# Kernel optimization log

Hardware: AMD Instinct MI355X
Metric: run time of the kernel (lower is better)

## Reference

```python
import jax, jax.numpy as jnp
import numpy as np

IN_F = 512
OUT_F = 512
ALPHA = 0.2   # LeakyReLU negative slope
NEG_INF = -9e15


def setup_inputs() -> dict:
    key = jax.random.key(0)
    k1, k2, k3, k4 = jax.random.split(key, 4)
    B, S = 8, 2048
    hidden_state = jax.random.normal(k1, (B, S, IN_F), dtype=jnp.float32)
    adjacent_matrix = jax.random.uniform(k2, (B, S, S), dtype=jnp.float32)
    # nn.Linear weight (no bias): stored as [out, in] in torch; we keep [in, out] for x @ W
    bound = 1.0 / np.sqrt(IN_F)
    W = jax.random.uniform(k3, (IN_F, OUT_F), dtype=jnp.float32, minval=-bound, maxval=bound)
    # xavier_uniform with gain=1.414 on a: shape [2*out, 1]
    a_bound = 1.414 * np.sqrt(6.0 / (2 * OUT_F + 1))
    a = jax.random.uniform(k4, (2 * OUT_F, 1), dtype=jnp.float32, minval=-a_bound, maxval=a_bound)
    return {"hidden_state": hidden_state, "adjacent_matrix": adjacent_matrix, "W": W, "a": a}


def reference(hidden_state, adjacent_matrix, W, a):
    # Wh: [B, S, out]
    Wh = jnp.einsum('bsi,io->bso', hidden_state, W)
    # additive attention: Wh1 + Wh2^T -> [B, S, S]
    Wh1 = Wh @ a[:OUT_F, :]            # [B, S, 1]
    Wh2 = Wh @ a[OUT_F:, :]            # [B, S, 1]
    e = Wh1 + jnp.swapaxes(Wh2, 1, 2)  # [B, S, S]
    e = jax.nn.leaky_relu(e, negative_slope=ALPHA)
    attention = jnp.where(adjacent_matrix > 0.5, e, NEG_INF)
    # NOTE: original softmaxes over dim=1 (the *row* index), faithfully reproduced
    attention = jax.nn.softmax(attention, axis=1)
    # dropout is identity at inference (training=False)
    h_prime = jnp.einsum('bst,bto->bso', attention, Wh)
    return jax.nn.elu(h_prime)  # concat=True path
```

## Files before the change

### kernel.cpp

```cpp
#include <hip/hip_runtime.h>
#include <hip/hip_bf16.h>
#include <stdint.h>

#define SDIM 2048
#define BDIM 8
#define FDIM 512
constexpr float ALPHA = 0.2f;

typedef __attribute__((ext_vector_type(8))) short bf16x8;
typedef __attribute__((ext_vector_type(4))) float f32x4;

__device__ __forceinline__ unsigned short f2bf(float x) {
  __hip_bfloat16 h = __float2bfloat16(x);
  return *reinterpret_cast<unsigned short*>(&h);
}

__device__ __forceinline__ void gload_lds16(const void* g, void* l) {
  __builtin_amdgcn_global_load_lds(
      (const __attribute__((address_space(1))) unsigned int*)(uintptr_t)g,
      (__attribute__((address_space(3))) unsigned int*)(uintptr_t)l,
      16, 0, 0);
}

__global__ void k0_prep(const float* __restrict__ W, const float* __restrict__ a,
                        float* __restrict__ wa, __hip_bfloat16* __restrict__ WT) {
  int i = blockIdx.x;
  int lane = threadIdx.x;
  float s1 = 0.f, s2 = 0.f;
  for (int o = lane; o < FDIM; o += 64) {
    float w = W[i * FDIM + o];
    s1 += w * a[o];
    s2 += w * a[FDIM + o];
    WT[o * FDIM + i] = __float2bfloat16(w);
  }
  #pragma unroll
  for (int off = 32; off > 0; off >>= 1) {
    s1 += __shfl_down(s1, off);
    s2 += __shfl_down(s2, off);
  }
  if (lane == 0) { wa[i] = s1; wa[FDIM + i] = s2; }
}

__global__ __launch_bounds__(256) void k1_rows(const float* __restrict__ H,
                                               const float* __restrict__ wa,
                                               float* __restrict__ Wh1, float* __restrict__ Wh2,
                                               __hip_bfloat16* __restrict__ Hb) {
  int wid = threadIdx.x >> 6, lane = threadIdx.x & 63;
  long r = (long)blockIdx.x * 4 + wid;
  const float* hr = H + r * FDIM;
  float4 v0 = ((const float4*)hr)[lane];
  float4 v1 = ((const float4*)hr)[lane + 64];
  float4 wa10 = ((const float4*)wa)[lane];
  float4 wa11 = ((const float4*)wa)[lane + 64];
  float4 wa20 = ((const float4*)(wa + FDIM))[lane];
  float4 wa21 = ((const float4*)(wa + FDIM))[lane + 64];
  float s1 = v0.x*wa10.x + v0.y*wa10.y + v0.z*wa10.z + v0.w*wa10.w
           + v1.x*wa11.x + v1.y*wa11.y + v1.z*wa11.z + v1.w*wa11.w;
  float s2 = v0.x*wa20.x + v0.y*wa20.y + v0.z*wa20.z + v0.w*wa20.w
           + v1.x*wa21.x + v1.y*wa21.y + v1.z*wa21.z + v1.w*wa21.w;
  ushort4 u0 = { f2bf(v0.x), f2bf(v0.y), f2bf(v0.z), f2bf(v0.w) };
  ushort4 u1 = { f2bf(v1.x), f2bf(v1.y), f2bf(v1.z), f2bf(v1.w) };
  ushort4* hb = (ushort4*)(Hb + r * FDIM);
  hb[lane] = u0;
  hb[lane + 64] = u1;
  #pragma unroll
  for (int off = 32; off > 0; off >>= 1) {
    s1 += __shfl_down(s1, off);
    s2 += __shfl_down(s2, off);
  }
  if (lane == 0) { Wh1[r] = s1; Wh2[r] = s2; }
}

__global__ __launch_bounds__(256) void k2_z(const float* __restrict__ adj,
                                            const float* __restrict__ Wh1,
                                            const float* __restrict__ Wh2,
                                            float* __restrict__ Zp) {
  int t = blockIdx.x * 256 + threadIdx.x;
  int b = blockIdx.y;
  int c = blockIdx.z;
  float w2 = Wh2[b * SDIM + t];
  const float* arow = adj + ((long)b * SDIM + c * 64) * SDIM + t;
  const float* w1p = Wh1 + b * SDIM + c * 64;
  float z = 0.f;
  #pragma unroll 8
  for (int s = 0; s < 64; ++s) {
    float av = arow[(long)s * SDIM];
    float e = w1p[s] + w2;
    e = e > 0.f ? e : ALPHA * e;
    float p = __expf(e);
    z += (av > 0.5f) ? p : 0.f;
  }
  Zp[(b * 32 + c) * SDIM + t] = z;
}

__global__ void k2b_rz(const float* __restrict__ Zp, float* __restrict__ rZ) {
  int idx = blockIdx.x * 256 + threadIdx.x;
  int b = idx >> 11, t = idx & 2047;
  float z = 0.f;
  #pragma unroll
  for (int c = 0; c < 32; ++c) z += Zp[(b * 32 + c) * SDIM + t];
  rZ[idx] = 1.0f / z;
}

__global__ __launch_bounds__(256) void k3_gemm(const __hip_bfloat16* __restrict__ WTm,
                                               const __hip_bfloat16* __restrict__ Hb,
                                               const float* __restrict__ rZ,
                                               __hip_bfloat16* __restrict__ VT) {
  __shared__ __align__(16) __hip_bfloat16 Asm[2][128 * 32];
  __shared__ __align__(16) __hip_bfloat16 Bsm[2][128 * 32];
  const int o0 = blockIdx.x * 128;
  const int t0 = blockIdx.y * 128;
  const int b = blockIdx.z;
  const int tid = threadIdx.x;
  const int w = tid >> 6, lane = tid & 63;
  const int wm = w >> 1, wn = w & 1;
  const int fr = lane & 15, fq = lane >> 4;
  const int lr = lane >> 2, lb = (lane & 3) * 16;

  const __hip_bfloat16* Abase = WTm + (long)o0 * FDIM;
  const __hip_bfloat16* Bbase = Hb + ((long)b * SDIM + t0) * FDIM;

  f32x4 acc[4][4] = {};

  auto stage = [&](int kk, int buf) {
    #pragma unroll
    for (int g = 0; g < 2; ++g) {
      int rbase = g * 64 + w * 16;
      int row = rbase + lr;
      gload_lds16((const char*)(Abase + (long)row * FDIM + kk * 32) + lb,
                  (char*)&Asm[buf][0] + rbase * 64);
      gload_lds16((const char*)(Bbase + (long)row * FDIM + kk * 32) + lb,
                  (char*)&Bsm[buf][0] + rbase * 64);
    }
  };

  stage(0, 0);
  __syncthreads();
  for (int kk = 0; kk < 16; ++kk) {
    int cur = kk & 1;
    if (kk < 15) stage(kk + 1, cur ^ 1);
    bf16x8 af[4], bf_[4];
    #pragma unroll
    for (int mf = 0; mf < 4; ++mf)
      af[mf] = *(const bf16x8*)((const char*)&Asm[cur][0] + (wm * 64 + mf * 16 + fr) * 64 + fq * 16);
    #pragma unroll
    for (int nf = 0; nf < 4; ++nf)
      bf_[nf] = *(const bf16x8*)((const char*)&Bsm[cur][0] + (wn * 64 + nf * 16 + fr) * 64 + fq * 16);
    #pragma unroll
    for (int mf = 0; mf < 4; ++mf)
      #pragma unroll
      for (int nf = 0; nf < 4; ++nf)
        acc[mf][nf] = __builtin_amdgcn_mfma_f32_16x16x32_bf16(af[mf], bf_[nf], acc[mf][nf], 0, 0, 0);
    __syncthreads();
  }

  #pragma unroll
  for (int nf = 0; nf < 4; ++nf) {
    int t = t0 + wn * 64 + nf * 16 + fr;
    float rz = rZ[b * SDIM + t];
    #pragma unroll
    for (int mf = 0; mf < 4; ++mf) {
      #pragma unroll
      for (int r = 0; r < 4; ++r) {
        int o = o0 + wm * 64 + mf * 16 + fq * 4 + r;
        VT[((long)(b * FDIM + o)) * SDIM + t] = __float2bfloat16(acc[mf][nf][r] * rz);
      }
    }
  }
}

__global__ __launch_bounds__(256, 2) void k4_pv(const float* __restrict__ adj,
                                                const float* __restrict__ Wh1,
                                                const float* __restrict__ Wh2,
                                                const __hip_bfloat16* __restrict__ VT,
                                                float* __restrict__ out) {
  __shared__ __align__(16) __hip_bfloat16 Vsm[2][256 * 32];
  __shared__ __align__(16) float AdjSm[3][64 * 32];
  __shared__ __align__(16) __hip_bfloat16 Psm[2][64 * 32];
  __shared__ __align__(16) float w2l[SDIM];
  const int b  = blockIdx.x;
  const int s0 = blockIdx.y * 64;
  const int ob = blockIdx.z * 256;
  const int tid = threadIdx.x;
  const int w = tid >> 6, lane = tid & 63;
  const int fr = lane & 15, fq = lane >> 4;
  const int sl = tid >> 2, oct = tid & 3;
  const int chk = (oct + sl) & 3;

  const float w1 = Wh1[b * SDIM + s0 + sl];
  const char* adjG = (const char*)(adj + ((long)b * SDIM + s0) * SDIM);
  const char* vtG  = (const char*)(VT + ((long)(b * FDIM + ob)) * SDIM);
  const char* w2G  = (const char*)(Wh2 + (long)b * SDIM);

  f32x4 acc[4][4] = {};

  auto stageV = [&](int p, int buf) {
    #pragma unroll
    for (int g = 0; g < 4; ++g) {
      int row = w * 64 + g * 16 + (lane >> 2);
      gload_lds16(vtG + ((long)row * SDIM + p * 32) * 2 + (lane & 3) * 16,
                  (char*)&Vsm[buf][0] + (w * 64 + g * 16) * 64);
    }
  };
  auto stageA = [&](int p, int slot) {
    #pragma unroll
    for (int g = 0; g < 2; ++g) {
      int row = w * 16 + g * 8 + (lane >> 3);
      gload_lds16(adjG + ((long)row * SDIM + p * 32) * 4 + (lane & 7) * 16,
                  (char*)&AdjSm[slot][0] + (w * 16 + g * 8) * 128);
    }
  };
  auto build = [&](int p, int pbuf, int slot) {
    const float* arow = &AdjSm[slot][sl * 32 + chk * 8];
    float4 a0 = *(const float4*)(arow);
    float4 a1 = *(const float4*)(arow + 4);
    const float* wrow = &w2l[p * 32 + chk * 8];
    float4 q0 = *(const float4*)(wrow);
    float4 q1 = *(const float4*)(wrow + 4);
    float aa[8] = {a0.x,a0.y,a0.z,a0.w,a1.x,a1.y,a1.z,a1.w};
    float qq[8] = {q0.x,q0.y,q0.z,q0.w,q1.x,q1.y,q1.z,q1.w};
    bf16x8 pv;
    #pragma unroll
    for (int i = 0; i < 8; ++i) {
      float e = w1 + qq[i];
      e = fmaxf(e, ALPHA * e);
      float pr = (aa[i] > 0.5f) ? __expf(e) : 0.f;
      pv[i] = (short)f2bf(pr);
    }
    *(bf16x8*)(&Psm[pbuf][sl * 32 + chk * 8]) = pv;
  };

  #pragma unroll
  for (int g = 0; g < 2; ++g)
    gload_lds16(w2G + w * 2048 + g * 1024 + lane * 16,
                (char*)w2l + w * 2048 + g * 1024);
  stageA(0, 0);
  stageA(1, 1);
  stageV(0, 0);
  asm volatile("s_waitcnt vmcnt(0)" ::: "memory");
  __syncthreads();
  build(0, 0, 0);
  stageA(2, 2);
  asm volatile("s_waitcnt lgkmcnt(0)" ::: "memory");
  __builtin_amdgcn_sched_barrier(0);
  __builtin_amdgcn_s_barrier();

  int slotS = 0;
  int slotB = 1;
  for (int p = 0; p < 64; ++p) {
    const int cur = p & 1;
    if (p <= 62) stageV(p + 1, cur ^ 1);
    if (p <= 60) stageA(p + 3, slotS);
    __builtin_amdgcn_sched_barrier(0);

    bf16x8 pa[4], vb[4];
    #pragma unroll
    for (int mf = 0; mf < 4; ++mf)
      pa[mf] = *(const bf16x8*)(&Psm[cur][(mf * 16 + fr) * 32 + fq * 8]);
    #pragma unroll
    for (int nf = 0; nf < 4; ++nf)
      vb[nf] = *(const bf16x8*)(&Vsm[cur][(w * 64 + nf * 16 + fr) * 32 + fq * 8]);
    __builtin_amdgcn_s_setprio(1);
    #pragma unroll
    for (int mf = 0; mf < 4; ++mf)
      #pragma unroll
      for (int nf = 0; nf < 4; ++nf)
        acc[mf][nf] = __builtin_amdgcn_mfma_f32_16x16x32_bf16(pa[mf], vb[nf], acc[mf][nf], 0, 0, 0);
    __builtin_amdgcn_s_setprio(0);

    if (p <= 62) build(p + 1, cur ^ 1, slotB);

    if (p <= 60) { asm volatile("s_waitcnt vmcnt(2)" ::: "memory"); }
    else         { asm volatile("s_waitcnt vmcnt(0)" ::: "memory"); }
    asm volatile("s_waitcnt lgkmcnt(0)" ::: "memory");
    __builtin_amdgcn_sched_barrier(0);
    __builtin_amdgcn_s_barrier();

    slotS = slotB;
    slotB = (slotB == 2) ? 0 : slotB + 1;
  }

  float* orow = out + ((long)b * SDIM + s0) * FDIM + ob + w * 64;
  #pragma unroll
  for (int mf = 0; mf < 4; ++mf) {
    #pragma unroll
    for (int nf = 0; nf < 4; ++nf) {
      #pragma unroll
      for (int r = 0; r < 4; ++r) {
        int s = mf * 16 + fq * 4 + r;
        int o = nf * 16 + fr;
        float x = acc[mf][nf][r];
        x = x > 0.f ? x : (__expf(x) - 1.f);
        orow[(long)s * FDIM + o] = x;
      }
    }
  }
}

extern "C" void kernel_launch(void* const* d_in, const int* in_sizes, int n_in,
                              void* d_out, int out_size, void* d_ws, size_t ws_size,
                              hipStream_t stream) {
  const float* H   = (const float*)d_in[0];
  const float* adj = (const float*)d_in[1];
  const float* W   = (const float*)d_in[2];
  const float* a   = (const float*)d_in[3];
  float* out = (float*)d_out;
  char* ws = (char*)d_ws;

  __hip_bfloat16* VT  = (__hip_bfloat16*)(ws + 0);
  __hip_bfloat16* Hb  = (__hip_bfloat16*)(ws + 16777216);
  __hip_bfloat16* WT  = (__hip_bfloat16*)(ws + 33554432);
  float* wa  = (float*)(ws + 34078720);
  float* Wh1 = (float*)(ws + 34082816);
  float* Wh2 = (float*)(ws + 34148352);
  float* rZ  = (float*)(ws + 34213888);
  float* Zp  = (float*)(ws + 34279424);

  hipLaunchKernelGGL(k0_prep, dim3(512), dim3(64), 0, stream, W, a, wa, WT);
  hipLaunchKernelGGL(k1_rows, dim3(4096), dim3(256), 0, stream, H, wa, Wh1, Wh2, Hb);
  hipLaunchKernelGGL(k2_z, dim3(8, 8, 32), dim3(256), 0, stream, adj, Wh1, Wh2, Zp);
  hipLaunchKernelGGL(k2b_rz, dim3(64), dim3(256), 0, stream, Zp, rZ);
  hipLaunchKernelGGL(k3_gemm, dim3(4, 16, 8), dim3(256), 0, stream, WT, Hb, rZ, VT);
  hipLaunchKernelGGL(k4_pv, dim3(8, 32, 2), dim3(256), 0, stream, adj, Wh1, Wh2, VT, out);
}
```

Before: 125.4 us.

## Store LDS tiles in MFMA fragment order to make loads lane-contiguous

Changes the global-to-LDS staging of V, adjacency and P tiles so each lane's 16-byte chunk lands at lane*16 within a fragment-ordered block. MFMA operand reads and the P build then become fully contiguous per wave, which avoids LDS bank conflicts from the old row-major layout with its strided fragment reads. The cost is less coalesced global loads: each lane now fetches a 16-byte piece from a different row, with 64-byte (V) or 128-byte (adjacency) contiguous runs per row instead of full rows.

Result: slower. 149.1 us (+18.9%).

```diff
diff --git a/kernel.cpp b/kernel.cpp
--- a/kernel.cpp
+++ b/kernel.cpp
@@ -184,10 +184,11 @@
   const int tid = threadIdx.x;
   const int w = tid >> 6, lane = tid & 63;
   const int fr = lane & 15, fq = lane >> 4;
-  const int sl = tid >> 2, oct = tid & 3;
-  const int chk = (oct + sl) & 3;
-
-  const float w1 = Wh1[b * SDIM + s0 + sl];
+
+  const int brow = w * 16 + (lane & 15);
+  const int bchk = lane >> 4;
+
+  const float w1 = Wh1[b * SDIM + s0 + brow];
   const char* adjG = (const char*)(adj + ((long)b * SDIM + s0) * SDIM);
   const char* vtG  = (const char*)(VT + ((long)(b * FDIM + ob)) * SDIM);
   const char* w2G  = (const char*)(Wh2 + (long)b * SDIM);
@@ -197,24 +198,22 @@
   auto stageV = [&](int p, int buf) {
     #pragma unroll
     for (int g = 0; g < 4; ++g) {
-      int row = w * 64 + g * 16 + (lane >> 2);
-      gload_lds16(vtG + ((long)row * SDIM + p * 32) * 2 + (lane & 3) * 16,
-                  (char*)&Vsm[buf][0] + (w * 64 + g * 16) * 64);
+      int row = w * 64 + g * 16 + (lane & 15);
+      gload_lds16(vtG + ((long)row * SDIM + p * 32 + (lane >> 4) * 8) * 2,
+                  (char*)&Vsm[buf][0] + w * 4096 + g * 1024);
     }
   };
   auto stageA = [&](int p, int slot) {
-    #pragma unroll
-    for (int g = 0; g < 2; ++g) {
-      int row = w * 16 + g * 8 + (lane >> 3);
-      gload_lds16(adjG + ((long)row * SDIM + p * 32) * 4 + (lane & 7) * 16,
-                  (char*)&AdjSm[slot][0] + (w * 16 + g * 8) * 128);
-    }
+    int row = w * 16 + (lane & 15);
+    const char* src = adjG + ((long)row * SDIM + p * 32 + (lane >> 4) * 8) * 4;
+    gload_lds16(src,      (char*)&AdjSm[slot][0] + w * 2048);
+    gload_lds16(src + 16, (char*)&AdjSm[slot][0] + w * 2048 + 1024);
   };
   auto build = [&](int p, int pbuf, int slot) {
-    const float* arow = &AdjSm[slot][sl * 32 + chk * 8];
-    float4 a0 = *(const float4*)(arow);
-    float4 a1 = *(const float4*)(arow + 4);
-    const float* wrow = &w2l[p * 32 + chk * 8];
+    const char* abase = (const char*)&AdjSm[slot][0] + w * 2048 + lane * 16;
+    float4 a0 = *(const float4*)(abase);
+    float4 a1 = *(const float4*)(abase + 1024);
+    const float* wrow = &w2l[p * 32 + bchk * 8];
     float4 q0 = *(const float4*)(wrow);
     float4 q1 = *(const float4*)(wrow + 4);
     float aa[8] = {a0.x,a0.y,a0.z,a0.w,a1.x,a1.y,a1.z,a1.w};
@@ -227,7 +226,7 @@
       float pr = (aa[i] > 0.5f) ? __expf(e) : 0.f;
       pv[i] = (short)f2bf(pr);
     }
-    *(bf16x8*)(&Psm[pbuf][sl * 32 + chk * 8]) = pv;
+    *(bf16x8*)((char*)&Psm[pbuf][0] + w * 1024 + lane * 16) = pv;
   };
 
   #pragma unroll
@@ -256,10 +255,10 @@
     bf16x8 pa[4], vb[4];
     #pragma unroll
     for (int mf = 0; mf < 4; ++mf)
-      pa[mf] = *(const bf16x8*)(&Psm[cur][(mf * 16 + fr) * 32 + fq * 8]);
+      pa[mf] = *(const bf16x8*)((const char*)&Psm[cur][0] + mf * 1024 + lane * 16);
     #pragma unroll
     for (int nf = 0; nf < 4; ++nf)
-      vb[nf] = *(const bf16x8*)(&Vsm[cur][(w * 64 + nf * 16 + fr) * 32 + fq * 8]);
+      vb[nf] = *(const bf16x8*)((const char*)&Vsm[cur][0] + w * 4096 + nf * 1024 + lane * 16);
     __builtin_amdgcn_s_setprio(1);
     #pragma unroll
     for (int mf = 0; mf < 4; ++mf)
```
